# Kernel tuning notes

Hardware: AMD Instinct MI355X
Metric: run time of the kernel (lower is better)

The kernel has to match this reference:

```python
import jax, jax.numpy as jnp
import numpy as np

B, N, H, E = 64, 512, 32, 4
N_STEPS = 5
ANNO = 1


def setup_inputs() -> dict:
    key = jax.random.key(0)
    ks = jax.random.split(key, 20)
    sc_h = 1.0 / np.sqrt(H)
    sc_3h = 1.0 / np.sqrt(3 * H)
    sc_ha = 1.0 / np.sqrt(H + ANNO)
    inp = {
        "x": jax.random.normal(ks[0], (B, N, H), jnp.float32),
        "a": jax.random.uniform(ks[1], (B, N, ANNO), jnp.float32),
        "m": jax.random.uniform(ks[2], (B, N, 2 * N * E), jnp.float32),
        # fc_in / fc_out: hidden -> hidden*n_edge (torch Linear: W [out,in])
        "W_in": jax.random.normal(ks[3], (H * E, H), jnp.float32) * sc_h,
        "b_in": jax.random.normal(ks[4], (H * E,), jnp.float32) * sc_h,
        "W_out": jax.random.normal(ks[5], (H * E, H), jnp.float32) * sc_h,
        "b_out": jax.random.normal(ks[6], (H * E,), jnp.float32) * sc_h,
        # GRU-style gates: 3*hidden -> hidden
        "Wz": jax.random.normal(ks[7], (H, 3 * H), jnp.float32) * sc_3h,
        "bz": jax.random.normal(ks[8], (H,), jnp.float32) * sc_3h,
        "Wr": jax.random.normal(ks[9], (H, 3 * H), jnp.float32) * sc_3h,
        "br": jax.random.normal(ks[10], (H,), jnp.float32) * sc_3h,
        "Wt": jax.random.normal(ks[11], (H, 3 * H), jnp.float32) * sc_3h,
        "bt": jax.random.normal(ks[12], (H,), jnp.float32) * sc_3h,
        # output head (task_id not in {18,19}): fc1, fc2
        "W1": jax.random.normal(ks[13], (H, H + ANNO), jnp.float32) * sc_ha,
        "b1": jax.random.normal(ks[14], (H,), jnp.float32) * sc_ha,
        "W2": jax.random.normal(ks[15], (1, H), jnp.float32) * sc_h,
        "b2": jax.random.normal(ks[16], (1,), jnp.float32) * sc_h,
    }
    return inp


def _reorder(s):
    # [B, N, H*E] -> view(B,N,H,E) -> transpose(2,3) -> transpose(1,2) -> [B, E*N, H]
    return s.reshape(B, N, H, E).transpose(0, 3, 1, 2).reshape(B, E * N, H)


def reference(x, a, m, W_in, b_in, W_out, b_out, Wz, bz, Wr, br, Wt, bt, W1, b1, W2, b2):
    m_in = m[:, :, : N * E]   # [B, N, N*E]
    m_out = m[:, :, N * E :]  # [B, N, N*E]
    h = x
    for _ in range(N_STEPS):
        s_in = _reorder(h @ W_in.T + b_in)    # [B, E*N, H]
        s_out = _reorder(h @ W_out.T + b_out)  # [B, E*N, H]
        a_in = jnp.einsum("bnm,bmh->bnh", m_in, s_in)
        a_out = jnp.einsum("bnm,bmh->bnh", m_out, s_out)
        cat = jnp.concatenate([a_in, a_out, h], axis=-1)  # [B, N, 3H]
        z = jax.nn.sigmoid(cat @ Wz.T + bz)
        r = jax.nn.sigmoid(cat @ Wr.T + br)
        joint = jnp.concatenate([a_in, a_out, r * h], axis=-1)
        h_hat = jnp.tanh(joint @ Wt.T + bt)
        h = (1.0 - z) * h + z * h_hat
    out = jnp.tanh(jnp.concatenate([h, a], axis=-1) @ W1.T + b1)  # [B, N, H]
    out = (out @ W2.T + b2).sum(-1)  # [B, N]
    return out
```

## Files before the change

### kernel.cpp

```cpp
#include <hip/hip_runtime.h>
#include <hip/hip_fp16.h>
#include <math.h>

#define B_ 64
#define N_ 512
#define H_ 32
#define E_ 4
#define NSTEPS 5
#define KTOT 2048

typedef _Float16 half8 __attribute__((ext_vector_type(8)));
typedef float   f32x4 __attribute__((ext_vector_type(4)));

__device__ __forceinline__ void gld16(const void* g, void* l) {
    __builtin_amdgcn_global_load_lds(
        (const __attribute__((address_space(1))) void*)g,
        (__attribute__((address_space(3))) void*)l, 16, 0, 0);
}

#define ABUF 16384
#define HBUF 8192
#define BBUF 8192
__global__ __launch_bounds__(256) void k_es(const float* __restrict__ m,
                                            const float* __restrict__ hsrc,
                                            const float* __restrict__ W_in,
                                            const float* __restrict__ b_in,
                                            const float* __restrict__ W_out,
                                            const float* __restrict__ b_out,
                                            float* __restrict__ a_in,
                                            float* __restrict__ a_out,
                                            int rev) {
    __shared__ __align__(16) char lds[2 * ABUF + 2 * HBUF + 2 * BBUF];
    int flat = blockIdx.x + (blockIdx.y << 3) + (blockIdx.z << 9);
    if (rev) flat = 1023 - flat;
    int nblk = flat & 7;
    int b    = (flat >> 3) & 63;
    int dir  = flat >> 9;
    int n0   = nblk * 64;
    int tid  = threadIdx.x;
    int w    = tid >> 6;
    int lane = tid & 63;
    int l15  = lane & 15;
    int quad = lane >> 4;
    int hu   = __builtin_amdgcn_readfirstlane(tid >> 6);

    const char* mBase = (const char*)(m + ((size_t)(b * N_ + n0)) * (2 * KTOT)
                                        + (size_t)dir * KTOT);
    const char* hB = (const char*)(hsrc + (size_t)b * N_ * H_);
    const float* Wf  = dir ? W_out : W_in;
    const float* bfp = dir ? b_out : b_in;
    float* aout = dir ? a_out : a_in;

    auto STAGE = [&](int c, int buf) {
        char* dA = lds + buf * ABUF;
        char* dH = lds + 2 * ABUF + buf * HBUF;
#pragma unroll
        for (int i = 0; i < 4; i++) {
            int r = (w << 4) + i * 4 + (lane >> 4);
            const char* g = mBase + (size_t)r * (2 * KTOT * 4) + c * 256
                            + (((lane & 15) * 16) ^ ((r & 7) << 4));
            gld16(g, dA + ((w << 4) + i * 4) * 256);
        }
        int hrow0 = (c & 7) * 64;
#pragma unroll
        for (int i = 0; i < 2; i++) {
            int rl = lane >> 3, pp = lane & 7;
            const char* g = hB + (size_t)(hrow0 + w * 16 + i * 8 + rl) * 128
                            + ((pp ^ (rl & 7)) * 16);
            gld16(g, dH + w * 2048 + i * 1024);
        }
    };

    f32x4 acc0 = {0.f,0.f,0.f,0.f}, acc1 = {0.f,0.f,0.f,0.f};

    int rowA  = (w << 4) + l15;
    int swzA  = (rowA & 7) << 4;
    int swzB0 = (l15 & 7) << 4;

    STAGE(0, 0);

    for (int c = 0; c < 32; c++) {
        int buf = c & 1;
        if (c < 31) STAGE(c + 1, buf ^ 1);
        if (c < 31) asm volatile("s_waitcnt vmcnt(6)" ::: "memory");
        else        asm volatile("s_waitcnt vmcnt(0)" ::: "memory");
        __builtin_amdgcn_s_barrier();
        __builtin_amdgcn_sched_barrier(0);

        char* Bb = lds + 2 * ABUF + 2 * HBUF + buf * BBUF;

        {
            const char* hC = lds + 2 * ABUF + buf * HBUF;
            int j = lane;
            f32x4 hv[8];
#pragma unroll
            for (int u = 0; u < 8; u++)
                hv[u] = *(const f32x4*)(hC + j * 128 + ((u ^ (j & 7)) * 16));
            int e = c >> 3;
#pragma unroll
            for (int i = 0; i < 8; i++) {
                int hr = hu * 8 + i;
                int he = hr * 4 + e;
                const f32x4* wr = (const f32x4*)(Wf + (size_t)he * H_);
                float acc = bfp[he];
#pragma unroll
                for (int c8 = 0; c8 < 8; c8++) {
                    f32x4 wv = wr[c8];
                    acc += hv[c8][0]*wv[0] + hv[c8][1]*wv[1]
                         + hv[c8][2]*wv[2] + hv[c8][3]*wv[3];
                }
                _Float16 hi = (_Float16)acc;
                _Float16 lo = (_Float16)(acc - (float)hi);
                int byte = hr * 128 + ((j * 2) ^ ((hr & 7) << 4));
                *(_Float16*)(Bb + byte)        = hi;
                *(_Float16*)(Bb + 4096 + byte) = lo;
            }
        }
        asm volatile("s_waitcnt lgkmcnt(0)" ::: "memory");
        __builtin_amdgcn_sched_barrier(0);
        __builtin_amdgcn_s_barrier();
        __builtin_amdgcn_sched_barrier(0);

        const char* Ab = lds + buf * ABUF + rowA * 256;
        const char* Bh = Bb;
        const char* Bl = Bb + 4096;
#pragma unroll
        for (int it = 0; it < 2; it++) {
            int kab = it * 128 + quad * 32;
            f32x4 a0 = *(const f32x4*)(Ab + (kab ^ swzA));
            f32x4 a1 = *(const f32x4*)(Ab + ((kab + 16) ^ swzA));

            int kbb = it * 64 + quad * 16;
            int o0 = l15 * 128        + (kbb ^ swzB0);
            int o1 = (l15 + 16) * 128 + (kbb ^ swzB0);
            half8 Bhi0 = *(const half8*)(Bh + o0);
            half8 Bhi1 = *(const half8*)(Bh + o1);
            half8 Blo0 = *(const half8*)(Bl + o0);
            half8 Blo1 = *(const half8*)(Bl + o1);

            half8 Ahi, Alo;
#pragma unroll
            for (int jj = 0; jj < 4; jj++) {
                float v0 = a0[jj], v1 = a1[jj];
                _Float16 h0 = (_Float16)v0, h1 = (_Float16)v1;
                Ahi[jj]     = h0;
                Ahi[jj + 4] = h1;
                Alo[jj]     = (_Float16)(v0 - (float)h0);
                Alo[jj + 4] = (_Float16)(v1 - (float)h1);
            }
            acc0 = __builtin_amdgcn_mfma_f32_16x16x32_f16(Ahi, Bhi0, acc0, 0, 0, 0);
            acc1 = __builtin_amdgcn_mfma_f32_16x16x32_f16(Ahi, Bhi1, acc1, 0, 0, 0);
            acc0 = __builtin_amdgcn_mfma_f32_16x16x32_f16(Ahi, Blo0, acc0, 0, 0, 0);
            acc1 = __builtin_amdgcn_mfma_f32_16x16x32_f16(Ahi, Blo1, acc1, 0, 0, 0);
            acc0 = __builtin_amdgcn_mfma_f32_16x16x32_f16(Alo, Bhi0, acc0, 0, 0, 0);
            acc1 = __builtin_amdgcn_mfma_f32_16x16x32_f16(Alo, Bhi1, acc1, 0, 0, 0);
        }
    }

#pragma unroll
    for (int r = 0; r < 4; r++) {
        size_t rr = (size_t)b * N_ + (n0 + w * 16 + quad * 4 + r);
        aout[rr * H_ + l15]      = acc0[r];
        aout[rr * H_ + 16 + l15] = acc1[r];
    }
}

__global__ __launch_bounds__(256) void k_gate(const float* __restrict__ a_in,
                                              const float* __restrict__ a_out,
                                              const float* __restrict__ hold_src,
                                              float* __restrict__ hstate,
                                              const float* __restrict__ Wz,
                                              const float* __restrict__ bz,
                                              const float* __restrict__ Wr,
                                              const float* __restrict__ br,
                                              const float* __restrict__ Wt,
                                              const float* __restrict__ bt) {
    __shared__ float cat[8][96];
    __shared__ float rh[8][32];
    int base = blockIdx.x * 8;
    int t = threadIdx.x;

    for (int idx = t; idx < 768; idx += 256) {
        int r = idx / 96, c = idx - r * 96;
        size_t row = (size_t)(base + r);
        float v;
        if (c < 32)      v = a_in [row * 32 + c];
        else if (c < 64) v = a_out[row * 32 + (c - 32)];
        else             v = hold_src[row * 32 + (c - 64)];
        cat[r][c] = v;
    }
    __syncthreads();

    int r = t >> 5, i = t & 31;
    float az = bz[i], ar = br[i];
    const f32x4* wzr = (const f32x4*)(Wz + (size_t)i * 96);
    const f32x4* wrr = (const f32x4*)(Wr + (size_t)i * 96);
    const f32x4* crow = (const f32x4*)cat[r];
#pragma unroll
    for (int kc = 0; kc < 24; kc++) {
        f32x4 cv = crow[kc];
        f32x4 wz = wzr[kc];
        f32x4 wr = wrr[kc];
        az += cv[0]*wz[0] + cv[1]*wz[1] + cv[2]*wz[2] + cv[3]*wz[3];
        ar += cv[0]*wr[0] + cv[1]*wr[1] + cv[2]*wr[2] + cv[3]*wr[3];
    }
    float z  = 1.f / (1.f + __expf(-az));
    float rg = 1.f / (1.f + __expf(-ar));
    float hold = cat[r][64 + i];
    rh[r][i] = rg * hold;
    __syncthreads();

    float at = bt[i];
    const f32x4* wtr = (const f32x4*)(Wt + (size_t)i * 96);
#pragma unroll
    for (int kc = 0; kc < 16; kc++) {
        f32x4 cv = crow[kc];
        f32x4 wt = wtr[kc];
        at += cv[0]*wt[0] + cv[1]*wt[1] + cv[2]*wt[2] + cv[3]*wt[3];
    }
    const f32x4* rrow = (const f32x4*)rh[r];
#pragma unroll
    for (int kc = 0; kc < 8; kc++) {
        f32x4 cv = rrow[kc];
        f32x4 wt = wtr[16 + kc];
        at += cv[0]*wt[0] + cv[1]*wt[1] + cv[2]*wt[2] + cv[3]*wt[3];
    }
    float hh = tanhf(at);
    hstate[(size_t)(base + r) * 32 + i] = (1.f - z) * hold + z * hh;
}

__global__ __launch_bounds__(256) void k_final(const float* __restrict__ hstate,
                                               const float* __restrict__ a,
                                               const float* __restrict__ W1,
                                               const float* __restrict__ b1,
                                               const float* __restrict__ W2,
                                               const float* __restrict__ b2,
                                               float* __restrict__ out) {
    __shared__ float hl[8][32];
    __shared__ float as[8];
    int base = blockIdx.x * 8;
    int t = threadIdx.x;
    {
        int r = t >> 5, c = t & 31;
        hl[r][c] = hstate[(size_t)(base + r) * 32 + c];
        if (t < 8) as[t] = a[base + t];
    }
    __syncthreads();
    int r = t >> 5, j = t & 31;
    float acc = b1[j];
    const float* w1r = W1 + (size_t)j * 33;
#pragma unroll
    for (int i2 = 0; i2 < 32; i2++) acc += hl[r][i2] * w1r[i2];
    acc += as[r] * w1r[32];
    float o = tanhf(acc) * W2[j];
#pragma unroll
    for (int off = 16; off; off >>= 1) o += __shfl_xor(o, off, 32);
    if (j == 0) out[base + r] = o + b2[0];
}

extern "C" void kernel_launch(void* const* d_in, const int* in_sizes, int n_in,
                              void* d_out, int out_size, void* d_ws, size_t ws_size,
                              hipStream_t stream) {
    const float* x     = (const float*)d_in[0];
    const float* a     = (const float*)d_in[1];
    const float* m     = (const float*)d_in[2];
    const float* W_in  = (const float*)d_in[3];
    const float* b_in  = (const float*)d_in[4];
    const float* W_out = (const float*)d_in[5];
    const float* b_out = (const float*)d_in[6];
    const float* Wz    = (const float*)d_in[7];
    const float* bz    = (const float*)d_in[8];
    const float* Wr    = (const float*)d_in[9];
    const float* br    = (const float*)d_in[10];
    const float* Wt    = (const float*)d_in[11];
    const float* bt    = (const float*)d_in[12];
    const float* W1    = (const float*)d_in[13];
    const float* b1    = (const float*)d_in[14];
    const float* W2    = (const float*)d_in[15];
    const float* b2    = (const float*)d_in[16];
    float* out = (float*)d_out;

    char* ws = (char*)d_ws;
    float* h    = (float*)(ws);
    float* a_in = (float*)(ws + ((size_t)4 << 20));
    float* a_out= (float*)(ws + ((size_t)8 << 20));

    for (int s = 0; s < NSTEPS; s++) {
        const float* hsrc = (s == 0) ? x : h;
        k_es<<<dim3(8, 64, 2), 256, 0, stream>>>(m, hsrc, W_in, b_in,
                                                 W_out, b_out, a_in, a_out,
                                                 s & 1);
        k_gate<<<4096, 256, 0, stream>>>(a_in, a_out, hsrc, h,
                                         Wz, bz, Wr, br, Wt, bt);
    }
    k_final<<<4096, 256, 0, stream>>>(h, a, W1, b1, W2, b2, out);
}
```

Baseline: 2.147 ms.

## Merge in/out edge directions into one block looping over both halves

Each k_es block now handles both the incoming and outgoing edge directions for its (batch, 64-row) tile, running 64 chunk iterations instead of 32 and writing a_in at the midpoint. This halves the grid from 1024 to 512 blocks and keeps the double-buffered pipeline running across the direction switch, which cuts per-block prologue/epilogue overhead. The cost is half as many blocks to fill the GPU's compute units, which may reduce latency hiding and occupancy on a wide device.

```diff
diff --git a/kernel.cpp b/kernel.cpp
--- a/kernel.cpp
+++ b/kernel.cpp
@@ -31,11 +31,10 @@
                                             float* __restrict__ a_out,
                                             int rev) {
     __shared__ __align__(16) char lds[2 * ABUF + 2 * HBUF + 2 * BBUF];
-    int flat = blockIdx.x + (blockIdx.y << 3) + (blockIdx.z << 9);
-    if (rev) flat = 1023 - flat;
+    int flat = blockIdx.x + (blockIdx.y << 3);
+    if (rev) flat = 511 - flat;
     int nblk = flat & 7;
-    int b    = (flat >> 3) & 63;
-    int dir  = flat >> 9;
+    int b    = flat >> 3;
     int n0   = nblk * 64;
     int tid  = threadIdx.x;
     int w    = tid >> 6;
@@ -44,24 +43,24 @@
     int quad = lane >> 4;
     int hu   = __builtin_amdgcn_readfirstlane(tid >> 6);
 
-    const char* mBase = (const char*)(m + ((size_t)(b * N_ + n0)) * (2 * KTOT)
-                                        + (size_t)dir * KTOT);
+    const char* mRow = (const char*)(m + ((size_t)(b * N_ + n0)) * (2 * KTOT));
     const char* hB = (const char*)(hsrc + (size_t)b * N_ * H_);
-    const float* Wf  = dir ? W_out : W_in;
-    const float* bfp = dir ? b_out : b_in;
-    float* aout = dir ? a_out : a_in;
-
-    auto STAGE = [&](int c, int buf) {
+    const float* Wfd[2] = { W_in, W_out };
+    const float* bfd[2] = { b_in, b_out };
+
+    auto STAGE = [&](int cc, int buf) {
+        int dir_s = cc >> 5, c = cc & 31;
         char* dA = lds + buf * ABUF;
         char* dH = lds + 2 * ABUF + buf * HBUF;
+        const char* mD = mRow + dir_s * (KTOT * 4);
 #pragma unroll
         for (int i = 0; i < 4; i++) {
             int r = (w << 4) + i * 4 + (lane >> 4);
-            const char* g = mBase + (size_t)r * (2 * KTOT * 4) + c * 256
+            const char* g = mD + (size_t)r * (2 * KTOT * 4) + c * 256
                             + (((lane & 15) * 16) ^ ((r & 7) << 4));
             gld16(g, dA + ((w << 4) + i * 4) * 256);
         }
-        int hrow0 = (c & 7) * 64;
+        int hrow0 = (cc & 7) * 64;
 #pragma unroll
         for (int i = 0; i < 2; i++) {
             int rl = lane >> 3, pp = lane & 7;
@@ -79,15 +78,16 @@
 
     STAGE(0, 0);
 
-    for (int c = 0; c < 32; c++) {
-        int buf = c & 1;
-        if (c < 31) STAGE(c + 1, buf ^ 1);
-        if (c < 31) asm volatile("s_waitcnt vmcnt(6)" ::: "memory");
-        else        asm volatile("s_waitcnt vmcnt(0)" ::: "memory");
+    for (int cc = 0; cc < 64; cc++) {
+        int buf = cc & 1;
+        if (cc < 63) STAGE(cc + 1, buf ^ 1);
+        if (cc < 63) asm volatile("s_waitcnt vmcnt(6)" ::: "memory");
+        else         asm volatile("s_waitcnt vmcnt(0)" ::: "memory");
         __builtin_amdgcn_s_barrier();
         __builtin_amdgcn_sched_barrier(0);
 
         char* Bb = lds + 2 * ABUF + 2 * HBUF + buf * BBUF;
+        int dir_s = cc >> 5;
 
         {
             const char* hC = lds + 2 * ABUF + buf * HBUF;
@@ -96,7 +96,9 @@
 #pragma unroll
             for (int u = 0; u < 8; u++)
                 hv[u] = *(const f32x4*)(hC + j * 128 + ((u ^ (j & 7)) * 16));
-            int e = c >> 3;
+            int e = (cc >> 3) & 3;
+            const float* Wf  = Wfd[dir_s];
+            const float* bfp = bfd[dir_s];
 #pragma unroll
             for (int i = 0; i < 8; i++) {
                 int hr = hu * 8 + i;
@@ -155,13 +157,24 @@
             acc0 = __builtin_amdgcn_mfma_f32_16x16x32_f16(Alo, Bhi0, acc0, 0, 0, 0);
             acc1 = __builtin_amdgcn_mfma_f32_16x16x32_f16(Alo, Bhi1, acc1, 0, 0, 0);
         }
+
+        if (cc == 31) {
+#pragma unroll
+            for (int r = 0; r < 4; r++) {
+                size_t rr = (size_t)b * N_ + (n0 + w * 16 + quad * 4 + r);
+                a_in[rr * H_ + l15]      = acc0[r];
+                a_in[rr * H_ + 16 + l15] = acc1[r];
+            }
+            acc0 = (f32x4){0.f,0.f,0.f,0.f};
+            acc1 = (f32x4){0.f,0.f,0.f,0.f};
+        }
     }
 
 #pragma unroll
     for (int r = 0; r < 4; r++) {
         size_t rr = (size_t)b * N_ + (n0 + w * 16 + quad * 4 + r);
-        aout[rr * H_ + l15]      = acc0[r];
-        aout[rr * H_ + 16 + l15] = acc1[r];
+        a_out[rr * H_ + l15]      = acc0[r];
+        a_out[rr * H_ + 16 + l15] = acc1[r];
     }
 }
 
@@ -287,9 +300,9 @@
 
     for (int s = 0; s < NSTEPS; s++) {
         const float* hsrc = (s == 0) ? x : h;
-        k_es<<<dim3(8, 64, 2), 256, 0, stream>>>(m, hsrc, W_in, b_in,
-                                                 W_out, b_out, a_in, a_out,
-                                                 s & 1);
+        k_es<<<dim3(8, 64), 256, 0, stream>>>(m, hsrc, W_in, b_in,
+                                              W_out, b_out, a_in, a_out,
+                                              s & 1);
         k_gate<<<4096, 256, 0, stream>>>(a_in, a_out, hsrc, h,
                                          Wz, bz, Wr, br, Wt, bt);
     }
```

After: 3.094 ms. 44.1% more time.
